# Kernel optimization log

Measured on AMD Instinct MI355X. Metric: run time of the kernel, lower is better.

The kernel has to match this reference:

```python
import jax, jax.numpy as jnp
import numpy as np

B, L, N, D = 4096, 50, 50, 128
STD = 0.1


def setup_inputs() -> dict:
    key = jax.random.key(0)
    ks = jax.random.split(key, 6)
    seq_idx = jax.random.randint(ks[0], (B, L), 0, N, dtype=jnp.int32)
    mask = jnp.ones((B, L), dtype=jnp.int32)
    node_vectors = jax.random.normal(ks[1], (B, N, D), dtype=jnp.float32)
    u = lambda k, shp: jax.random.uniform(k, shp, jnp.float32, -STD, STD)
    return {
        "sequence_of_indexes": seq_idx,
        "mask": mask,
        "node_vectors": node_vectors,
        "batch_size": B,
        "W_last": u(ks[2], (D, D)),      # dense_last_item kernel (no bias)
        "W_seq": u(ks[3], (D, D)),       # dense_sequence_items kernel
        "b_seq": jnp.zeros((D,), jnp.float32),  # dense_sequence_items bias
        "W_alpha": u(ks[4], (D, 1)),     # dense_alpha kernel (no bias)
    }


def reference(sequence_of_indexes, mask, node_vectors, batch_size,
              W_last, W_seq, b_seq, W_alpha):
    maskf = mask.astype(jnp.float32)                          # [B, L]
    seq_len = jnp.sum(maskf, axis=1).astype(jnp.int32)        # [B]
    rows = jnp.arange(batch_size)
    # last item index per session, then gather its node vector
    last_idx = sequence_of_indexes[rows, seq_len - 1]         # [B]
    v_n = node_vectors[rows, last_idx]                        # [B, D]
    # per-batch embedding lookup: node_vectors[b, seq_idx[b]]
    v_i = jnp.take_along_axis(node_vectors, sequence_of_indexes[..., None], axis=1)  # [B, L, D]
    vn_proj = (v_n @ W_last)[:, None, :]                      # [B, 1, D]
    vi_proj = v_i @ W_seq + b_seq                             # [B, L, D]
    alpha = jax.nn.sigmoid(vn_proj + vi_proj) @ W_alpha       # [B, L, 1]
    alpha = alpha * maskf[..., None]
    session_graph = jnp.sum(alpha * v_i, axis=1)              # [B, D]
    return v_n, session_graph
```

## Files before the change

### kernel.cpp

```cpp
#include <hip/hip_runtime.h>
#include <math.h>

#define BB 4096
#define LL 50
#define NN 50
#define DD 128

typedef short bf16x8 __attribute__((ext_vector_type(8)));
typedef float f32x4  __attribute__((ext_vector_type(4)));

static __device__ inline unsigned short f32_to_bf16_rne(float f) {
    unsigned int u = __float_as_uint(f);
    u += 0x7FFFu + ((u >> 16) & 1u);
    return (unsigned short)(u >> 16);
}
static __device__ inline float bf16_to_f32(unsigned short h) {
    return __uint_as_float(((unsigned int)h) << 16);
}

__global__ void prep_w(const float* __restrict__ W_seq,
                       const float* __restrict__ W_last,
                       unsigned short* __restrict__ ws)
{
    int t = blockIdx.x * blockDim.x + threadIdx.x;
    int lane = t & 63;
    int nt   = (t >> 6) & 7;
    int kk   = t >> 9;
    const float* W = (kk < 4) ? W_seq : W_last;
    int kb = (kk & 3) * 32 + (lane >> 4) * 8;
    int n  = nt * 16 + (lane & 15);
    unsigned short* dst = ws + (size_t)t * 8;
    #pragma unroll
    for (int j = 0; j < 8; ++j)
        dst[j] = f32_to_bf16_rne(W[(kb + j) * DD + n]);
    (void)nt;
}

__global__ __launch_bounds__(256, 6) void sess_attn(
    const int*   __restrict__ seq_idx,
    const int*   __restrict__ mask,
    const float* __restrict__ nodes,
    const float* __restrict__ b_seq,
    const float* __restrict__ W_alpha,
    const unsigned short* __restrict__ wfrag,
    float*       __restrict__ out)
{
    const int b    = blockIdx.x;
    const int tid  = threadIdx.x;
    const int lane = tid & 63;
    const int wave = tid >> 6;
    const int col  = lane & 15;
    const int quad = lane >> 4;

    __shared__ __align__(16) unsigned short s_nbf[64][136];
    __shared__ float s_alpha[64];
    __shared__ float s_cntf[NN];
    __shared__ float s_b[DD];
    __shared__ float s_wa[DD];
    __shared__ int   s_last;

    if (tid < 64) s_alpha[tid] = 0.f;
    if (tid < NN) s_cntf[tid] = 0.f;
    if (tid < DD) { s_b[tid] = b_seq[tid]; s_wa[tid] = W_alpha[tid]; }

    const float* nb = nodes + (size_t)b * (NN * DD);
    for (int i = tid; i < NN * DD / 4; i += 256) {
        float4 v = ((const float4*)nb)[i];
        int r = i >> 5;
        int c = (i & 31) * 4;
        ushort4 h;
        h.x = f32_to_bf16_rne(v.x);
        h.y = f32_to_bf16_rne(v.y);
        h.z = f32_to_bf16_rne(v.z);
        h.w = f32_to_bf16_rne(v.w);
        *(ushort4*)&s_nbf[r][c] = h;
    }

    if (tid < 64) {
        int m = (tid < LL) ? mask[b * LL + tid] : 0;
        int mm = m;
        for (int off = 32; off; off >>= 1) mm += __shfl_down(mm, off);
        if (tid == 0) {
            int j = mm - 1;
            if (j < 0) j += LL;
            s_last = seq_idx[b * LL + j];
        }
        if (tid < LL && m) atomicAdd(&s_cntf[seq_idx[b * LL + tid]], (float)m);
    }
    __syncthreads();

    const int last = s_last;

    if (tid < DD) out[(size_t)b * DD + tid] = nb[last * DD + tid];

    f32x4 acc[4][2];
    #pragma unroll
    for (int m = 0; m < 4; ++m)
        #pragma unroll
        for (int j = 0; j < 2; ++j)
            acc[m][j] = (f32x4){0.f, 0.f, 0.f, 0.f};

    const bf16x8* wsf = (const bf16x8*)wfrag;
    #pragma unroll
    for (int kk = 0; kk < 8; ++kk) {
        bf16x8 a[4];
        if (kk < 4) {
            #pragma unroll
            for (int m = 0; m < 4; ++m)
                a[m] = *(const bf16x8*)&s_nbf[m * 16 + col][kk * 32 + quad * 8];
        } else {
            bf16x8 av = *(const bf16x8*)&s_nbf[last][(kk - 4) * 32 + quad * 8];
            a[0] = av; a[1] = av; a[2] = av; a[3] = av;
        }
        #pragma unroll
        for (int j = 0; j < 2; ++j) {
            bf16x8 bf = wsf[(size_t)((kk * 8 + (wave * 2 + j)) * 64 + lane)];
            #pragma unroll
            for (int m = 0; m < 4; ++m)
                acc[m][j] = __builtin_amdgcn_mfma_f32_16x16x32_bf16(a[m], bf, acc[m][j], 0, 0, 0);
        }
    }

    #pragma unroll
    for (int m = 0; m < 4; ++m) {
        float p[4] = {0.f, 0.f, 0.f, 0.f};
        #pragma unroll
        for (int j = 0; j < 2; ++j) {
            int n = (wave * 2 + j) * 16 + col;
            float bb = s_b[n];
            float wa = s_wa[n];
            #pragma unroll
            for (int r = 0; r < 4; ++r) {
                float x = acc[m][j][r] + bb;
                float sig = 1.f / (1.f + __expf(-x));
                p[r] = fmaf(sig, wa, p[r]);
            }
        }
        #pragma unroll
        for (int r = 0; r < 4; ++r) {
            float v = p[r];
            v += __shfl_xor(v, 1);
            v += __shfl_xor(v, 2);
            v += __shfl_xor(v, 4);
            v += __shfl_xor(v, 8);
            int row = m * 16 + quad * 4 + r;
            if (col == 0 && row < NN) atomicAdd(&s_alpha[row], v);
        }
    }
    __syncthreads();

    if (tid < DD) {
        float acc2 = 0.f;
        #pragma unroll 10
        for (int n = 0; n < NN; ++n)
            acc2 = fmaf(s_cntf[n] * s_alpha[n], bf16_to_f32(s_nbf[n][tid]), acc2);
        out[(size_t)BB * DD + (size_t)b * DD + tid] = acc2;
    }
}

extern "C" void kernel_launch(void* const* d_in, const int* in_sizes, int n_in,
                              void* d_out, int out_size, void* d_ws, size_t ws_size,
                              hipStream_t stream) {
    const int*   seq     = (const int*)  d_in[0];
    const int*   mask    = (const int*)  d_in[1];
    const float* nodes   = (const float*)d_in[2];
    const float* W_last  = (const float*)d_in[4];
    const float* W_seq   = (const float*)d_in[5];
    const float* b_seq   = (const float*)d_in[6];
    const float* W_alpha = (const float*)d_in[7];
    float*       out     = (float*)      d_out;

    unsigned short* wsf = (unsigned short*)d_ws;

    prep_w<<<16, 256, 0, stream>>>(W_seq, W_last, wsf);
    sess_attn<<<BB, 256, 0, stream>>>(seq, mask, nodes, b_seq, W_alpha, wsf, out);
}
```

Measured before the change: 195.8 us.

## Process four sessions per block with register-resident weight fragments and double-buffered LDS

Each block now handles four batch rows in a loop instead of one. The bf16 weight fragments are loaded into registers once and reused across those rows, and the mask and index loads for all rows are prefetched up front. Shared node buffers are ping-ponged so the next row's staging can start while earlier work on the other buffer drains. In exchange there are four times fewer blocks, which lowers parallelism, and the 16 extra register fragments raise register pressure (launch bounds drop to 4).

```diff
diff --git a/kernel.cpp b/kernel.cpp
--- a/kernel.cpp
+++ b/kernel.cpp
@@ -5,6 +5,7 @@
 #define LL 50
 #define NN 50
 #define DD 128
+#define GG 4
 
 typedef short bf16x8 __attribute__((ext_vector_type(8)));
 typedef float f32x4  __attribute__((ext_vector_type(4)));
@@ -33,10 +34,9 @@
     #pragma unroll
     for (int j = 0; j < 8; ++j)
         dst[j] = f32_to_bf16_rne(W[(kb + j) * DD + n]);
-    (void)nt;
 }
 
-__global__ __launch_bounds__(256, 6) void sess_attn(
+__global__ __launch_bounds__(256, 4) void sess_attn(
     const int*   __restrict__ seq_idx,
     const int*   __restrict__ mask,
     const float* __restrict__ nodes,
@@ -45,116 +45,138 @@
     const unsigned short* __restrict__ wfrag,
     float*       __restrict__ out)
 {
-    const int b    = blockIdx.x;
     const int tid  = threadIdx.x;
     const int lane = tid & 63;
     const int wave = tid >> 6;
     const int col  = lane & 15;
     const int quad = lane >> 4;
+    const int b0   = blockIdx.x * GG;
 
-    __shared__ __align__(16) unsigned short s_nbf[64][136];
-    __shared__ float s_alpha[64];
-    __shared__ float s_cntf[NN];
+    __shared__ __align__(16) unsigned short s_nbf[2][64][136];
+    __shared__ float s_alpha[2][64];
+    __shared__ float s_cntf[2][64];
     __shared__ float s_b[DD];
     __shared__ float s_wa[DD];
-    __shared__ int   s_last;
+    __shared__ int   s_last[2];
 
-    if (tid < 64) s_alpha[tid] = 0.f;
-    if (tid < NN) s_cntf[tid] = 0.f;
+    const bf16x8* wsf = (const bf16x8*)wfrag;
+    bf16x8 bfrag[16];
+    #pragma unroll
+    for (int kk = 0; kk < 8; ++kk)
+        #pragma unroll
+        for (int j = 0; j < 2; ++j)
+            bfrag[kk * 2 + j] = wsf[(size_t)((kk * 8 + wave * 2 + j) * 64 + lane)];
+
     if (tid < DD) { s_b[tid] = b_seq[tid]; s_wa[tid] = W_alpha[tid]; }
 
-    const float* nb = nodes + (size_t)b * (NN * DD);
-    for (int i = tid; i < NN * DD / 4; i += 256) {
-        float4 v = ((const float4*)nb)[i];
-        int r = i >> 5;
-        int c = (i & 31) * 4;
-        ushort4 h;
-        h.x = f32_to_bf16_rne(v.x);
-        h.y = f32_to_bf16_rne(v.y);
-        h.z = f32_to_bf16_rne(v.z);
-        h.w = f32_to_bf16_rne(v.w);
-        *(ushort4*)&s_nbf[r][c] = h;
-    }
-
+    int pm[GG], pi[GG];
     if (tid < 64) {
-        int m = (tid < LL) ? mask[b * LL + tid] : 0;
-        int mm = m;
-        for (int off = 32; off; off >>= 1) mm += __shfl_down(mm, off);
-        if (tid == 0) {
-            int j = mm - 1;
-            if (j < 0) j += LL;
-            s_last = seq_idx[b * LL + j];
-        }
-        if (tid < LL && m) atomicAdd(&s_cntf[seq_idx[b * LL + tid]], (float)m);
-    }
-    __syncthreads();
-
-    const int last = s_last;
-
-    if (tid < DD) out[(size_t)b * DD + tid] = nb[last * DD + tid];
-
-    f32x4 acc[4][2];
-    #pragma unroll
-    for (int m = 0; m < 4; ++m)
         #pragma unroll
-        for (int j = 0; j < 2; ++j)
-            acc[m][j] = (f32x4){0.f, 0.f, 0.f, 0.f};
-
-    const bf16x8* wsf = (const bf16x8*)wfrag;
-    #pragma unroll
-    for (int kk = 0; kk < 8; ++kk) {
-        bf16x8 a[4];
-        if (kk < 4) {
-            #pragma unroll
-            for (int m = 0; m < 4; ++m)
-                a[m] = *(const bf16x8*)&s_nbf[m * 16 + col][kk * 32 + quad * 8];
-        } else {
-            bf16x8 av = *(const bf16x8*)&s_nbf[last][(kk - 4) * 32 + quad * 8];
-            a[0] = av; a[1] = av; a[2] = av; a[3] = av;
-        }
-        #pragma unroll
-        for (int j = 0; j < 2; ++j) {
-            bf16x8 bf = wsf[(size_t)((kk * 8 + (wave * 2 + j)) * 64 + lane)];
-            #pragma unroll
-            for (int m = 0; m < 4; ++m)
-                acc[m][j] = __builtin_amdgcn_mfma_f32_16x16x32_bf16(a[m], bf, acc[m][j], 0, 0, 0);
+        for (int g = 0; g < GG; ++g) {
+            int bg = b0 + g;
+            pm[g] = (tid < LL) ? mask[bg * LL + tid]    : 0;
+            pi[g] = (tid < LL) ? seq_idx[bg * LL + tid] : 0;
         }
     }
 
-    #pragma unroll
-    for (int m = 0; m < 4; ++m) {
-        float p[4] = {0.f, 0.f, 0.f, 0.f};
+    for (int g = 0; g < GG; ++g) {
+        const int b = b0 + g;
+        const int p = g & 1;
+        const float* nb = nodes + (size_t)b * (NN * DD);
+
+        if (tid < 64) { s_alpha[p][tid] = 0.f; s_cntf[p][tid] = 0.f; }
+
+        for (int i = tid; i < NN * DD / 4; i += 256) {
+            float4 v = ((const float4*)nb)[i];
+            int r = i >> 5, c = (i & 31) * 4;
+            ushort4 h;
+            h.x = f32_to_bf16_rne(v.x);
+            h.y = f32_to_bf16_rne(v.y);
+            h.z = f32_to_bf16_rne(v.z);
+            h.w = f32_to_bf16_rne(v.w);
+            *(ushort4*)&s_nbf[p][r][c] = h;
+        }
+
+        if (tid < 64) {
+            int mm = pm[g];
+            mm += __shfl_xor(mm, 1);  mm += __shfl_xor(mm, 2);
+            mm += __shfl_xor(mm, 4);  mm += __shfl_xor(mm, 8);
+            mm += __shfl_xor(mm, 16); mm += __shfl_xor(mm, 32);
+            int j = mm - 1;
+            if (j < 0) j += LL;
+            int li = __shfl(pi[g], j);
+            if (tid == 0) s_last[p] = li;
+            if (tid < LL && pm[g]) atomicAdd(&s_cntf[p][pi[g]], (float)pm[g]);
+        }
+        __syncthreads();
+
+        const int last = s_last[p];
+
+        if (tid < DD) out[(size_t)b * DD + tid] = nb[last * DD + tid];
+
+        f32x4 acc[4][2];
         #pragma unroll
-        for (int j = 0; j < 2; ++j) {
-            int n = (wave * 2 + j) * 16 + col;
-            float bb = s_b[n];
-            float wa = s_wa[n];
+        for (int m = 0; m < 4; ++m)
+            #pragma unroll
+            for (int j = 0; j < 2; ++j)
+                acc[m][j] = (f32x4){0.f, 0.f, 0.f, 0.f};
+
+        #pragma unroll
+        for (int kk = 0; kk < 8; ++kk) {
+            bf16x8 a[4];
+            if (kk < 4) {
+                #pragma unroll
+                for (int m = 0; m < 4; ++m)
+                    a[m] = *(const bf16x8*)&s_nbf[p][m * 16 + col][kk * 32 + quad * 8];
+            } else {
+                bf16x8 av = *(const bf16x8*)&s_nbf[p][last][(kk - 4) * 32 + quad * 8];
+                a[0] = av; a[1] = av; a[2] = av; a[3] = av;
+            }
+            #pragma unroll
+            for (int j = 0; j < 2; ++j) {
+                #pragma unroll
+                for (int m = 0; m < 4; ++m)
+                    acc[m][j] = __builtin_amdgcn_mfma_f32_16x16x32_bf16(
+                        a[m], bfrag[kk * 2 + j], acc[m][j], 0, 0, 0);
+            }
+        }
+
+        #pragma unroll
+        for (int m = 0; m < 4; ++m) {
+            float pr[4] = {0.f, 0.f, 0.f, 0.f};
+            #pragma unroll
+            for (int j = 0; j < 2; ++j) {
+                int n = (wave * 2 + j) * 16 + col;
+                float bb = s_b[n];
+                float wa = s_wa[n];
+                #pragma unroll
+                for (int r = 0; r < 4; ++r) {
+                    float x = acc[m][j][r] + bb;
+                    float sig = 1.f / (1.f + __expf(-x));
+                    pr[r] = fmaf(sig, wa, pr[r]);
+                }
+            }
             #pragma unroll
             for (int r = 0; r < 4; ++r) {
-                float x = acc[m][j][r] + bb;
-                float sig = 1.f / (1.f + __expf(-x));
-                p[r] = fmaf(sig, wa, p[r]);
+                float v = pr[r];
+                v += __shfl_xor(v, 1);
+                v += __shfl_xor(v, 2);
+                v += __shfl_xor(v, 4);
+                v += __shfl_xor(v, 8);
+                int row = m * 16 + quad * 4 + r;
+                if (col == 0 && row < NN) atomicAdd(&s_alpha[p][row], v);
             }
         }
-        #pragma unroll
-        for (int r = 0; r < 4; ++r) {
-            float v = p[r];
-            v += __shfl_xor(v, 1);
-            v += __shfl_xor(v, 2);
-            v += __shfl_xor(v, 4);
-            v += __shfl_xor(v, 8);
-            int row = m * 16 + quad * 4 + r;
-            if (col == 0 && row < NN) atomicAdd(&s_alpha[row], v);
+        __syncthreads();
+
+        if (tid < DD) {
+            float acc2 = 0.f;
+            #pragma unroll 10
+            for (int n = 0; n < NN; ++n)
+                acc2 = fmaf(s_cntf[p][n] * s_alpha[p][n],
+                            bf16_to_f32(s_nbf[p][n][tid]), acc2);
+            out[(size_t)BB * DD + (size_t)b * DD + tid] = acc2;
         }
-    }
-    __syncthreads();
-
-    if (tid < DD) {
-        float acc2 = 0.f;
-        #pragma unroll 10
-        for (int n = 0; n < NN; ++n)
-            acc2 = fmaf(s_cntf[n] * s_alpha[n], bf16_to_f32(s_nbf[n][tid]), acc2);
-        out[(size_t)BB * DD + (size_t)b * DD + tid] = acc2;
     }
 }
 
@@ -173,5 +195,5 @@
     unsigned short* wsf = (unsigned short*)d_ws;
 
     prep_w<<<16, 256, 0, stream>>>(W_seq, W_last, wsf);
-    sess_attn<<<BB, 256, 0, stream>>>(seq, mask, nodes, b_seq, W_alpha, wsf, out);
+    sess_attn<<<BB / GG, 256, 0, stream>>>(seq, mask, nodes, b_seq, W_alpha, wsf, out);
 }
```

Measured after the change: 216.9 us. 1.11x slower.

## Prefetch node tile and weight fragments into registers, separate last-item MFMA accumulator

Applied to the files above, without the earlier changes.

All global loads (node tile, weight fragments, mask/indices, bias and alpha weights) are issued up front into registers before any shared-memory work, so their latencies overlap. The last-item projection gets its own accumulator seeded with the bias instead of redundantly accumulating into all four M tiles, cutting MFMA count from 64 to 40 per wave. The mask reduction uses xor shuffles and a shuffle to fetch the last index. Register pressure rises sharply, so launch bounds drop to 3 blocks per SIMD, which lowers occupancy.

```diff
diff --git a/kernel.cpp b/kernel.cpp
--- a/kernel.cpp
+++ b/kernel.cpp
@@ -5,6 +5,7 @@
 #define LL 50
 #define NN 50
 #define DD 128
+#define STR 136
 
 typedef short bf16x8 __attribute__((ext_vector_type(8)));
 typedef float f32x4  __attribute__((ext_vector_type(4)));
@@ -33,10 +34,9 @@
     #pragma unroll
     for (int j = 0; j < 8; ++j)
         dst[j] = f32_to_bf16_rne(W[(kb + j) * DD + n]);
-    (void)nt;
-}
-
-__global__ __launch_bounds__(256, 6) void sess_attn(
+}
+
+__global__ __launch_bounds__(256, 3) void sess_attn(
     const int*   __restrict__ seq_idx,
     const int*   __restrict__ mask,
     const float* __restrict__ nodes,
@@ -52,46 +52,82 @@
     const int col  = lane & 15;
     const int quad = lane >> 4;
 
-    __shared__ __align__(16) unsigned short s_nbf[64][136];
+    __shared__ __align__(16) unsigned short s_nbf[64][STR];
     __shared__ float s_alpha[64];
-    __shared__ float s_cntf[NN];
-    __shared__ float s_b[DD];
-    __shared__ float s_wa[DD];
+    __shared__ float s_cntf[64];
     __shared__ int   s_last;
 
-    if (tid < 64) s_alpha[tid] = 0.f;
-    if (tid < NN) s_cntf[tid] = 0.f;
-    if (tid < DD) { s_b[tid] = b_seq[tid]; s_wa[tid] = W_alpha[tid]; }
-
-    const float* nb = nodes + (size_t)b * (NN * DD);
-    for (int i = tid; i < NN * DD / 4; i += 256) {
-        float4 v = ((const float4*)nb)[i];
-        int r = i >> 5;
-        int c = (i & 31) * 4;
+    const float4* nb4 = (const float4*)(nodes + (size_t)b * (NN * DD));
+    float4 v[7];
+    #pragma unroll
+    for (int j = 0; j < 6; ++j) v[j] = nb4[tid + j * 256];
+    if (tid < 64) v[6] = nb4[tid + 1536];
+
+    const bf16x8* wsf = (const bf16x8*)wfrag;
+    bf16x8 bfS[8], bfL[8];
+    #pragma unroll
+    for (int kk = 0; kk < 4; ++kk)
+        #pragma unroll
+        for (int j = 0; j < 2; ++j) {
+            bfS[kk * 2 + j] = wsf[(size_t)(((kk    ) * 8 + wave * 2 + j) * 64 + lane)];
+            bfL[kk * 2 + j] = wsf[(size_t)(((kk + 4) * 8 + wave * 2 + j) * 64 + lane)];
+        }
+
+    int pm = 0, pi = 0;
+    if (tid < 64) {
+        pm = (tid < LL) ? mask[b * LL + tid]    : 0;
+        pi = (tid < LL) ? seq_idx[b * LL + tid] : 0;
+    }
+
+    float bb_r[2], wa_r[2];
+    #pragma unroll
+    for (int j = 0; j < 2; ++j) {
+        int n = (wave * 2 + j) * 16 + col;
+        bb_r[j] = b_seq[n];
+        wa_r[j] = W_alpha[n];
+    }
+
+    if (tid < 64) { s_alpha[tid] = 0.f; s_cntf[tid] = 0.f; }
+
+    #pragma unroll
+    for (int j = 0; j < 6; ++j) {
+        int idx = tid + j * 256;
+        int r = idx >> 5, c = (idx & 31) * 4;
         ushort4 h;
-        h.x = f32_to_bf16_rne(v.x);
-        h.y = f32_to_bf16_rne(v.y);
-        h.z = f32_to_bf16_rne(v.z);
-        h.w = f32_to_bf16_rne(v.w);
+        h.x = f32_to_bf16_rne(v[j].x);
+        h.y = f32_to_bf16_rne(v[j].y);
+        h.z = f32_to_bf16_rne(v[j].z);
+        h.w = f32_to_bf16_rne(v[j].w);
         *(ushort4*)&s_nbf[r][c] = h;
     }
-
     if (tid < 64) {
-        int m = (tid < LL) ? mask[b * LL + tid] : 0;
-        int mm = m;
-        for (int off = 32; off; off >>= 1) mm += __shfl_down(mm, off);
-        if (tid == 0) {
-            int j = mm - 1;
-            if (j < 0) j += LL;
-            s_last = seq_idx[b * LL + j];
-        }
-        if (tid < LL && m) atomicAdd(&s_cntf[seq_idx[b * LL + tid]], (float)m);
+        int idx = tid + 1536;
+        int r = idx >> 5, c = (idx & 31) * 4;
+        ushort4 h;
+        h.x = f32_to_bf16_rne(v[6].x);
+        h.y = f32_to_bf16_rne(v[6].y);
+        h.z = f32_to_bf16_rne(v[6].z);
+        h.w = f32_to_bf16_rne(v[6].w);
+        *(ushort4*)&s_nbf[r][c] = h;
+    }
+
+    if (tid < 64) {
+        int mm = pm;
+        mm += __shfl_xor(mm, 1);  mm += __shfl_xor(mm, 2);
+        mm += __shfl_xor(mm, 4);  mm += __shfl_xor(mm, 8);
+        mm += __shfl_xor(mm, 16); mm += __shfl_xor(mm, 32);
+        int j = mm - 1;
+        if (j < 0) j += LL;
+        int li = __shfl(pi, j);
+        if (tid == 0) s_last = li;
+        if (tid < LL && pm) atomicAdd(&s_cntf[pi], (float)pm);
     }
     __syncthreads();
 
     const int last = s_last;
 
-    if (tid < DD) out[(size_t)b * DD + tid] = nb[last * DD + tid];
+    if (tid < DD)
+        out[(size_t)b * DD + tid] = nodes[(size_t)b * (NN * DD) + last * DD + tid];
 
     f32x4 acc[4][2];
     #pragma unroll
@@ -99,52 +135,51 @@
         #pragma unroll
         for (int j = 0; j < 2; ++j)
             acc[m][j] = (f32x4){0.f, 0.f, 0.f, 0.f};
-
-    const bf16x8* wsf = (const bf16x8*)wfrag;
-    #pragma unroll
-    for (int kk = 0; kk < 8; ++kk) {
+    f32x4 accV[2];
+    #pragma unroll
+    for (int j = 0; j < 2; ++j)
+        accV[j] = (f32x4){bb_r[j], bb_r[j], bb_r[j], bb_r[j]};
+
+    #pragma unroll
+    for (int kk = 0; kk < 4; ++kk) {
         bf16x8 a[4];
-        if (kk < 4) {
+        #pragma unroll
+        for (int m = 0; m < 4; ++m)
+            a[m] = *(const bf16x8*)&s_nbf[m * 16 + col][kk * 32 + quad * 8];
+        bf16x8 av = *(const bf16x8*)&s_nbf[last][kk * 32 + quad * 8];
+        #pragma unroll
+        for (int j = 0; j < 2; ++j) {
             #pragma unroll
             for (int m = 0; m < 4; ++m)
-                a[m] = *(const bf16x8*)&s_nbf[m * 16 + col][kk * 32 + quad * 8];
-        } else {
-            bf16x8 av = *(const bf16x8*)&s_nbf[last][(kk - 4) * 32 + quad * 8];
-            a[0] = av; a[1] = av; a[2] = av; a[3] = av;
-        }
+                acc[m][j] = __builtin_amdgcn_mfma_f32_16x16x32_bf16(
+                    a[m], bfS[kk * 2 + j], acc[m][j], 0, 0, 0);
+            accV[j] = __builtin_amdgcn_mfma_f32_16x16x32_bf16(
+                av, bfL[kk * 2 + j], accV[j], 0, 0, 0);
+        }
+    }
+
+    #pragma unroll
+    for (int m = 0; m < 4; ++m) {
+        float pr[4] = {0.f, 0.f, 0.f, 0.f};
         #pragma unroll
         for (int j = 0; j < 2; ++j) {
-            bf16x8 bf = wsf[(size_t)((kk * 8 + (wave * 2 + j)) * 64 + lane)];
-            #pragma unroll
-            for (int m = 0; m < 4; ++m)
-                acc[m][j] = __builtin_amdgcn_mfma_f32_16x16x32_bf16(a[m], bf, acc[m][j], 0, 0, 0);
-        }
-    }
-
-    #pragma unroll
-    for (int m = 0; m < 4; ++m) {
-        float p[4] = {0.f, 0.f, 0.f, 0.f};
-        #pragma unroll
-        for (int j = 0; j < 2; ++j) {
-            int n = (wave * 2 + j) * 16 + col;
-            float bb = s_b[n];
-            float wa = s_wa[n];
+            float wa = wa_r[j];
             #pragma unroll
             for (int r = 0; r < 4; ++r) {
-                float x = acc[m][j][r] + bb;
+                float x = acc[m][j][r] + accV[j][r];
                 float sig = 1.f / (1.f + __expf(-x));
-                p[r] = fmaf(sig, wa, p[r]);
+                pr[r] = fmaf(sig, wa, pr[r]);
             }
         }
         #pragma unroll
         for (int r = 0; r < 4; ++r) {
-            float v = p[r];
-            v += __shfl_xor(v, 1);
-            v += __shfl_xor(v, 2);
-            v += __shfl_xor(v, 4);
-            v += __shfl_xor(v, 8);
+            float vv = pr[r];
+            vv += __shfl_xor(vv, 1);
+            vv += __shfl_xor(vv, 2);
+            vv += __shfl_xor(vv, 4);
+            vv += __shfl_xor(vv, 8);
             int row = m * 16 + quad * 4 + r;
-            if (col == 0 && row < NN) atomicAdd(&s_alpha[row], v);
+            if (col == 0 && row < NN) atomicAdd(&s_alpha[row], vv);
         }
     }
     __syncthreads();
```

Measured after the change: 177.3 us. 9.4% less time.
